# Performance work log

Measured on AMD Instinct MI355X. Metric: run time of the kernel, lower is better.

Reference implementation:

```python
import jax, jax.numpy as jnp
import numpy as np

B, C, D = 512, 1000, 512
K = 10


def setup_inputs() -> dict:
    key = jax.random.key(0)
    k1, k2, k3, k4, k5 = jax.random.split(key, 5)
    x = jax.random.normal(k1, (B, D), dtype=jnp.float32)
    protos = jax.random.normal(k2, (C, D), dtype=jnp.float32)
    # ex2/ex1 chosen so N*ex2^2 - ex1^2 > 0 (valid sqrt)
    ex2 = jax.random.uniform(k3, (C, D), dtype=jnp.float32) + 1.0
    ex1 = jax.random.uniform(k4, (C, D), dtype=jnp.float32) * 0.1
    cls_num = jax.random.randint(k5, (C,), 1, 100, dtype=jnp.int32)
    proto_label = jnp.arange(C, dtype=jnp.int32)
    return {"x": x, "protos": protos, "ex2": ex2, "ex1": ex1,
            "cls_num": cls_num, "proto_label": proto_label, "k_nearest": K}


def reference(x, protos, ex2, ex1, cls_num, proto_label, k_nearest):
    # rd: per-class, per-feature variance proxy  [C, D]
    N = cls_num[:, None].astype(ex2.dtype)
    rd = jnp.sqrt(N * ex2 ** 2 - ex1 ** 2)
    # softmax over feature dim of (rowmax - rd)
    rd = jax.nn.softmax(jnp.max(rd, axis=1, keepdims=True) - rd, axis=1)
    # weighted squared distances: [B, C, D] -> reduce D -> [B, C]
    diff = x[:, None, :] - protos[None, :, :]
    x_dists = diff ** 2 * rd[None, :, :]
    simi_mat = x_dists.sum(axis=2)  # [B, C]
    # k smallest distances (torch.topk largest=False)
    neg_vals, topk_index = jax.lax.top_k(-simi_mat, k_nearest)
    topk_vals = -neg_vals  # [B, K]
    topk_conf = topk_vals.sum(axis=1, keepdims=True) / topk_vals  # [B, K]
    # pick prototype with max confidence, map through label table
    temp = jnp.argmax(topk_conf, axis=1)  # [B]
    ans_index = jnp.take_along_axis(topk_index, temp[:, None], axis=1)[:, 0]
    predict = proto_label[ans_index]  # [B]
    return predict, topk_conf
```

## Files before the change

kernel.cpp:

```cpp
#include <hip/hip_runtime.h>
#include <math.h>
#include <float.h>

#define B_SZ 512
#define C_SZ 1000
#define D_SZ 512
#define K_TOP 10
#define K2 1024
#define NSPLIT 4
#define KSPLIT (K2 / NSPLIT)
#define BC (B_SZ * C_SZ)

#define A_OFF   0
#define W_OFF   (B_SZ * K2)
#define T3_OFF  (W_OFF + C_SZ * K2)
#define PART_OFF (T3_OFF + 1024)

__global__ __launch_bounds__(256) void prep_kernel(const float* __restrict__ x,
                                                   const float* __restrict__ protos,
                                                   const float* __restrict__ ex2,
                                                   const float* __restrict__ ex1,
                                                   const int* __restrict__ cls_num,
                                                   float* __restrict__ ws) {
    float* A  = ws + A_OFF;
    float* W  = ws + W_OFF;
    float* t3 = ws + T3_OFF;
    const int wid  = threadIdx.x >> 6;
    const int lane = threadIdx.x & 63;
    const int blk  = blockIdx.x;

    if (blk < C_SZ / 4) {
        const int c = blk * 4 + wid;
        const size_t rb = (size_t)c * D_SZ + lane * 8;
        float e2v[8], e1v[8], pv[8];
        *(float4*)&e2v[0] = *(const float4*)(ex2 + rb);
        *(float4*)&e2v[4] = *(const float4*)(ex2 + rb + 4);
        *(float4*)&e1v[0] = *(const float4*)(ex1 + rb);
        *(float4*)&e1v[4] = *(const float4*)(ex1 + rb + 4);
        *(float4*)&pv[0]  = *(const float4*)(protos + rb);
        *(float4*)&pv[4]  = *(const float4*)(protos + rb + 4);
        const float N = (float)cls_num[c];

        float v[8], mn = FLT_MAX;
        #pragma unroll
        for (int k = 0; k < 8; k++) {
            v[k] = sqrtf(N * e2v[k] * e2v[k] - e1v[k] * e1v[k]);
            mn = fminf(mn, v[k]);
        }
        #pragma unroll
        for (int off = 1; off < 64; off <<= 1) mn = fminf(mn, __shfl_xor(mn, off));

        float ev[8], s = 0.f;
        #pragma unroll
        for (int k = 0; k < 8; k++) { ev[k] = expf(mn - v[k]); s += ev[k]; }
        #pragma unroll
        for (int off = 1; off < 64; off <<= 1) s += __shfl_xor(s, off);
        const float inv = 1.0f / s;

        float w1[8], w2[8], t = 0.f;
        #pragma unroll
        for (int k = 0; k < 8; k++) {
            const float rdv = ev[k] * inv;
            w1[k] = rdv;
            w2[k] = -2.0f * rdv * pv[k];
            t = fmaf(rdv * pv[k], pv[k], t);
        }
        float* wr = W + (size_t)c * K2 + lane * 8;
        *(float4*)(wr)              = *(float4*)&w1[0];
        *(float4*)(wr + 4)          = *(float4*)&w1[4];
        *(float4*)(wr + D_SZ)       = *(float4*)&w2[0];
        *(float4*)(wr + D_SZ + 4)   = *(float4*)&w2[4];
        #pragma unroll
        for (int off = 1; off < 64; off <<= 1) t += __shfl_xor(t, off);
        if (lane == 0) t3[c] = t;
    } else {
        const int b = (blk - C_SZ / 4) * 4 + wid;
        const size_t rb = (size_t)b * D_SZ + lane * 8;
        float xv[8], xs[8];
        *(float4*)&xv[0] = *(const float4*)(x + rb);
        *(float4*)&xv[4] = *(const float4*)(x + rb + 4);
        #pragma unroll
        for (int k = 0; k < 8; k++) xs[k] = xv[k] * xv[k];
        float* ar = A + (size_t)b * K2 + lane * 8;
        *(float4*)(ar)            = *(float4*)&xs[0];
        *(float4*)(ar + 4)        = *(float4*)&xs[4];
        *(float4*)(ar + D_SZ)     = *(float4*)&xv[0];
        *(float4*)(ar + D_SZ + 4) = *(float4*)&xv[4];
    }
}

#define TM 64
#define TN 64
#define KB 32

__global__ __launch_bounds__(256) void gemm_kernel(const float* __restrict__ A,
                                                   const float* __restrict__ W,
                                                   float* __restrict__ part) {
    __shared__ float as[KB][TM + 4];
    __shared__ float wsm[KB][TN + 4];

    const int tid = threadIdx.x;
    const int tx = tid & 15;
    const int ty = tid >> 4;
    const int c0 = blockIdx.x * TN;
    const int b0 = blockIdx.y * TM;
    const int kz = blockIdx.z;

    float acc[4][4] = {};

    for (int k0 = kz * KSPLIT; k0 < (kz + 1) * KSPLIT; k0 += KB) {
        #pragma unroll
        for (int i = 0; i < 2; i++) {
            const int f = tid + i * 256;
            const int row = f >> 3;
            const int col = (f & 7) * 4;
            float4 va = *(const float4*)(A + (size_t)(b0 + row) * K2 + k0 + col);
            as[col + 0][row] = va.x; as[col + 1][row] = va.y;
            as[col + 2][row] = va.z; as[col + 3][row] = va.w;
            const int cc = c0 + row;
            float4 vw = make_float4(0.f, 0.f, 0.f, 0.f);
            if (cc < C_SZ) vw = *(const float4*)(W + (size_t)cc * K2 + k0 + col);
            wsm[col + 0][row] = vw.x; wsm[col + 1][row] = vw.y;
            wsm[col + 2][row] = vw.z; wsm[col + 3][row] = vw.w;
        }
        __syncthreads();

        #pragma unroll
        for (int kk = 0; kk < KB; kk++) {
            float4 av4 = *(const float4*)&as[kk][ty * 4];
            float4 wv4 = *(const float4*)&wsm[kk][tx * 4];
            const float a[4] = {av4.x, av4.y, av4.z, av4.w};
            const float w[4] = {wv4.x, wv4.y, wv4.z, wv4.w};
            #pragma unroll
            for (int i = 0; i < 4; i++)
                #pragma unroll
                for (int j = 0; j < 4; j++)
                    acc[i][j] = fmaf(a[i], w[j], acc[i][j]);
        }
        __syncthreads();
    }

    float* o = part + (size_t)kz * BC;
    #pragma unroll
    for (int i = 0; i < 4; i++) {
        const int b = b0 + ty * 4 + i;
        const int c = c0 + tx * 4;
        if (c + 3 < C_SZ) {
            float4 v = {acc[i][0], acc[i][1], acc[i][2], acc[i][3]};
            *(float4*)(o + (size_t)b * C_SZ + c) = v;
        } else {
            #pragma unroll
            for (int j = 0; j < 4; j++)
                if (c + j < C_SZ) o[(size_t)b * C_SZ + c + j] = acc[i][j];
        }
    }
}

__global__ __launch_bounds__(256) void topk_kernel(const float* __restrict__ ws,
                                                   const int* __restrict__ proto_label,
                                                   float* __restrict__ out) {
    const float* part = ws + PART_OFF;
    const float* t3   = ws + T3_OFF;
    const int wid = threadIdx.x >> 6;
    const int lane = threadIdx.x & 63;
    const int b = blockIdx.x * 4 + wid;

    float vals[16];
    #pragma unroll
    for (int j = 0; j < 16; j++) {
        const int c = lane + j * 64;
        if (c < C_SZ) {
            const size_t idx = (size_t)b * C_SZ + c;
            vals[j] = t3[c] + part[idx] + part[BC + idx]
                    + part[2 * (size_t)BC + idx] + part[3 * (size_t)BC + idx];
        } else {
            vals[j] = FLT_MAX;
        }
    }

    float kv[K_TOP];
    int ki[K_TOP];
    for (int t = 0; t < K_TOP; t++) {
        float bv = FLT_MAX;
        int bi = 0x7fffffff;
        #pragma unroll
        for (int j = 0; j < 16; j++) {
            const int c = lane + j * 64;
            if (vals[j] < bv) { bv = vals[j]; bi = c; }
        }
        #pragma unroll
        for (int off = 1; off < 64; off <<= 1) {
            const float ov = __shfl_xor(bv, off);
            const int oi = __shfl_xor(bi, off);
            if (ov < bv || (ov == bv && oi < bi)) { bv = ov; bi = oi; }
        }
        kv[t] = bv;
        ki[t] = bi;
        if ((bi & 63) == lane) vals[bi >> 6] = FLT_MAX;
    }

    if (lane == 0) {
        float S = 0.f;
        #pragma unroll
        for (int t = 0; t < K_TOP; t++) S += kv[t];
        float conf[K_TOP];
        #pragma unroll
        for (int t = 0; t < K_TOP; t++) {
            conf[t] = S / kv[t];
            out[B_SZ + b * K_TOP + t] = conf[t];
        }
        int best = 0;
        for (int t = 1; t < K_TOP; t++)
            if (conf[t] > conf[best]) best = t;
        out[b] = (float)proto_label[ki[best]];
    }
}

extern "C" void kernel_launch(void* const* d_in, const int* in_sizes, int n_in,
                              void* d_out, int out_size, void* d_ws, size_t ws_size,
                              hipStream_t stream) {
    const float* x           = (const float*)d_in[0];
    const float* protos      = (const float*)d_in[1];
    const float* ex2         = (const float*)d_in[2];
    const float* ex1         = (const float*)d_in[3];
    const int*   cls_num     = (const int*)d_in[4];
    const int*   proto_label = (const int*)d_in[5];

    float* ws  = (float*)d_ws;
    float* out = (float*)d_out;

    prep_kernel<<<C_SZ / 4 + B_SZ / 4, 256, 0, stream>>>(x, protos, ex2, ex1,
                                                         cls_num, ws);

    dim3 g2((C_SZ + TN - 1) / TN, B_SZ / TM, NSPLIT);
    gemm_kernel<<<g2, 256, 0, stream>>>(ws + A_OFF, ws + W_OFF, ws + PART_OFF);

    topk_kernel<<<B_SZ / 4, 256, 0, stream>>>(ws, proto_label, out);
}
```

Before: 108.3 us.

## Fuse x-squaring into GEMM loads, prefetch tiles, and double split-K

The prep kernel no longer builds the augmented A matrix [x^2 | x]. The GEMM now reads x directly and squares it on the fly for the first half of the K splits, which removes a 2 MB write and re-read through workspace. The GEMM loop also register-prefetches the next chunk of x and W while computing the current one, and split-K goes from 4 to 8 for more blocks. In exchange, the top-k kernel must read and sum twice as many partial buffers.

```diff
diff --git a/kernel.cpp b/kernel.cpp
--- a/kernel.cpp
+++ b/kernel.cpp
@@ -7,94 +7,75 @@
 #define D_SZ 512
 #define K_TOP 10
 #define K2 1024
-#define NSPLIT 4
+#define NSPLIT 8
 #define KSPLIT (K2 / NSPLIT)
 #define BC (B_SZ * C_SZ)
 
-#define A_OFF   0
-#define W_OFF   (B_SZ * K2)
+#define W_OFF   0
 #define T3_OFF  (W_OFF + C_SZ * K2)
 #define PART_OFF (T3_OFF + 1024)
 
-__global__ __launch_bounds__(256) void prep_kernel(const float* __restrict__ x,
-                                                   const float* __restrict__ protos,
+__global__ __launch_bounds__(256) void prep_kernel(const float* __restrict__ protos,
                                                    const float* __restrict__ ex2,
                                                    const float* __restrict__ ex1,
                                                    const int* __restrict__ cls_num,
                                                    float* __restrict__ ws) {
-    float* A  = ws + A_OFF;
     float* W  = ws + W_OFF;
     float* t3 = ws + T3_OFF;
     const int wid  = threadIdx.x >> 6;
     const int lane = threadIdx.x & 63;
-    const int blk  = blockIdx.x;
-
-    if (blk < C_SZ / 4) {
-        const int c = blk * 4 + wid;
-        const size_t rb = (size_t)c * D_SZ + lane * 8;
-        float e2v[8], e1v[8], pv[8];
-        *(float4*)&e2v[0] = *(const float4*)(ex2 + rb);
-        *(float4*)&e2v[4] = *(const float4*)(ex2 + rb + 4);
-        *(float4*)&e1v[0] = *(const float4*)(ex1 + rb);
-        *(float4*)&e1v[4] = *(const float4*)(ex1 + rb + 4);
-        *(float4*)&pv[0]  = *(const float4*)(protos + rb);
-        *(float4*)&pv[4]  = *(const float4*)(protos + rb + 4);
-        const float N = (float)cls_num[c];
-
-        float v[8], mn = FLT_MAX;
-        #pragma unroll
-        for (int k = 0; k < 8; k++) {
-            v[k] = sqrtf(N * e2v[k] * e2v[k] - e1v[k] * e1v[k]);
-            mn = fminf(mn, v[k]);
-        }
-        #pragma unroll
-        for (int off = 1; off < 64; off <<= 1) mn = fminf(mn, __shfl_xor(mn, off));
-
-        float ev[8], s = 0.f;
-        #pragma unroll
-        for (int k = 0; k < 8; k++) { ev[k] = expf(mn - v[k]); s += ev[k]; }
-        #pragma unroll
-        for (int off = 1; off < 64; off <<= 1) s += __shfl_xor(s, off);
-        const float inv = 1.0f / s;
-
-        float w1[8], w2[8], t = 0.f;
-        #pragma unroll
-        for (int k = 0; k < 8; k++) {
-            const float rdv = ev[k] * inv;
-            w1[k] = rdv;
-            w2[k] = -2.0f * rdv * pv[k];
-            t = fmaf(rdv * pv[k], pv[k], t);
-        }
-        float* wr = W + (size_t)c * K2 + lane * 8;
-        *(float4*)(wr)              = *(float4*)&w1[0];
-        *(float4*)(wr + 4)          = *(float4*)&w1[4];
-        *(float4*)(wr + D_SZ)       = *(float4*)&w2[0];
-        *(float4*)(wr + D_SZ + 4)   = *(float4*)&w2[4];
-        #pragma unroll
-        for (int off = 1; off < 64; off <<= 1) t += __shfl_xor(t, off);
-        if (lane == 0) t3[c] = t;
-    } else {
-        const int b = (blk - C_SZ / 4) * 4 + wid;
-        const size_t rb = (size_t)b * D_SZ + lane * 8;
-        float xv[8], xs[8];
-        *(float4*)&xv[0] = *(const float4*)(x + rb);
-        *(float4*)&xv[4] = *(const float4*)(x + rb + 4);
-        #pragma unroll
-        for (int k = 0; k < 8; k++) xs[k] = xv[k] * xv[k];
-        float* ar = A + (size_t)b * K2 + lane * 8;
-        *(float4*)(ar)            = *(float4*)&xs[0];
-        *(float4*)(ar + 4)        = *(float4*)&xs[4];
-        *(float4*)(ar + D_SZ)     = *(float4*)&xv[0];
-        *(float4*)(ar + D_SZ + 4) = *(float4*)&xv[4];
-    }
+    const int c = blockIdx.x * 4 + wid;
+
+    const size_t rb = (size_t)c * D_SZ + lane * 8;
+    float e2v[8], e1v[8], pv[8];
+    *(float4*)&e2v[0] = *(const float4*)(ex2 + rb);
+    *(float4*)&e2v[4] = *(const float4*)(ex2 + rb + 4);
+    *(float4*)&e1v[0] = *(const float4*)(ex1 + rb);
+    *(float4*)&e1v[4] = *(const float4*)(ex1 + rb + 4);
+    *(float4*)&pv[0]  = *(const float4*)(protos + rb);
+    *(float4*)&pv[4]  = *(const float4*)(protos + rb + 4);
+    const float N = (float)cls_num[c];
+
+    float v[8], mn = FLT_MAX;
+    #pragma unroll
+    for (int k = 0; k < 8; k++) {
+        v[k] = sqrtf(N * e2v[k] * e2v[k] - e1v[k] * e1v[k]);
+        mn = fminf(mn, v[k]);
+    }
+    #pragma unroll
+    for (int off = 1; off < 64; off <<= 1) mn = fminf(mn, __shfl_xor(mn, off));
+
+    float ev[8], s = 0.f;
+    #pragma unroll
+    for (int k = 0; k < 8; k++) { ev[k] = expf(mn - v[k]); s += ev[k]; }
+    #pragma unroll
+    for (int off = 1; off < 64; off <<= 1) s += __shfl_xor(s, off);
+    const float inv = 1.0f / s;
+
+    float w1[8], w2[8], t = 0.f;
+    #pragma unroll
+    for (int k = 0; k < 8; k++) {
+        const float rdv = ev[k] * inv;
+        w1[k] = rdv;
+        w2[k] = -2.0f * rdv * pv[k];
+        t = fmaf(rdv * pv[k], pv[k], t);
+    }
+    float* wr = W + (size_t)c * K2 + lane * 8;
+    *(float4*)(wr)            = *(float4*)&w1[0];
+    *(float4*)(wr + 4)        = *(float4*)&w1[4];
+    *(float4*)(wr + D_SZ)     = *(float4*)&w2[0];
+    *(float4*)(wr + D_SZ + 4) = *(float4*)&w2[4];
+    #pragma unroll
+    for (int off = 1; off < 64; off <<= 1) t += __shfl_xor(t, off);
+    if (lane == 0) t3[c] = t;
 }
 
 #define TM 64
 #define TN 64
 #define KB 32
 
-__global__ __launch_bounds__(256) void gemm_kernel(const float* __restrict__ A,
-                                                   const float* __restrict__ W,
+__global__ __launch_bounds__(256) void gemm_kernel(const float* __restrict__ x,
+                                                   const float* __restrict__ Wm,
                                                    float* __restrict__ part) {
     __shared__ float as[KB][TM + 4];
     __shared__ float wsm[KB][TN + 4];
@@ -106,29 +87,59 @@
     const int b0 = blockIdx.y * TM;
     const int kz = blockIdx.z;
 
+    const int row0 = tid >> 3;
+    const int row1 = row0 + 32;
+    const int col4 = (tid & 7) * 4;
+
+    const bool sq = (kz < NSPLIT / 2);
+    const int khalf = sq ? kz * KSPLIT : kz * KSPLIT - D_SZ;
+
     float acc[4][4] = {};
-
-    for (int k0 = kz * KSPLIT; k0 < (kz + 1) * KSPLIT; k0 += KB) {
-        #pragma unroll
-        for (int i = 0; i < 2; i++) {
-            const int f = tid + i * 256;
-            const int row = f >> 3;
-            const int col = (f & 7) * 4;
-            float4 va = *(const float4*)(A + (size_t)(b0 + row) * K2 + k0 + col);
-            as[col + 0][row] = va.x; as[col + 1][row] = va.y;
-            as[col + 2][row] = va.z; as[col + 3][row] = va.w;
-            const int cc = c0 + row;
-            float4 vw = make_float4(0.f, 0.f, 0.f, 0.f);
-            if (cc < C_SZ) vw = *(const float4*)(W + (size_t)cc * K2 + k0 + col);
-            wsm[col + 0][row] = vw.x; wsm[col + 1][row] = vw.y;
-            wsm[col + 2][row] = vw.z; wsm[col + 3][row] = vw.w;
-        }
+    float4 pa0, pa1, pw0, pw1;
+
+    {
+        const int k0 = khalf;
+        pa0 = *(const float4*)(x + (size_t)(b0 + row0) * D_SZ + k0 + col4);
+        pa1 = *(const float4*)(x + (size_t)(b0 + row1) * D_SZ + k0 + col4);
+        const int kw = kz * KSPLIT;
+        const int cc0 = c0 + row0, cc1 = c0 + row1;
+        pw0 = (cc0 < C_SZ) ? *(const float4*)(Wm + (size_t)cc0 * K2 + kw + col4)
+                           : make_float4(0.f, 0.f, 0.f, 0.f);
+        pw1 = (cc1 < C_SZ) ? *(const float4*)(Wm + (size_t)cc1 * K2 + kw + col4)
+                           : make_float4(0.f, 0.f, 0.f, 0.f);
+    }
+
+    #pragma unroll
+    for (int ch = 0; ch < KSPLIT / KB; ch++) {
+        float4 a0 = pa0, a1 = pa1;
+        if (sq) {
+            a0.x *= a0.x; a0.y *= a0.y; a0.z *= a0.z; a0.w *= a0.w;
+            a1.x *= a1.x; a1.y *= a1.y; a1.z *= a1.z; a1.w *= a1.w;
+        }
+        as[col4 + 0][row0] = a0.x; as[col4 + 1][row0] = a0.y;
+        as[col4 + 2][row0] = a0.z; as[col4 + 3][row0] = a0.w;
+        as[col4 + 0][row1] = a1.x; as[col4 + 1][row1] = a1.y;
+        as[col4 + 2][row1] = a1.z; as[col4 + 3][row1] = a1.w;
+        wsm[col4 + 0][row0] = pw0.x; wsm[col4 + 1][row0] = pw0.y;
+        wsm[col4 + 2][row0] = pw0.z; wsm[col4 + 3][row0] = pw0.w;
+        wsm[col4 + 0][row1] = pw1.x; wsm[col4 + 1][row1] = pw1.y;
+        wsm[col4 + 2][row1] = pw1.z; wsm[col4 + 3][row1] = pw1.w;
         __syncthreads();
 
+        if (ch + 1 < KSPLIT / KB) {
+            const int k0 = khalf + (ch + 1) * KB;
+            pa0 = *(const float4*)(x + (size_t)(b0 + row0) * D_SZ + k0 + col4);
+            pa1 = *(const float4*)(x + (size_t)(b0 + row1) * D_SZ + k0 + col4);
+            const int kw = kz * KSPLIT + (ch + 1) * KB;
+            const int cc0 = c0 + row0, cc1 = c0 + row1;
+            if (cc0 < C_SZ) pw0 = *(const float4*)(Wm + (size_t)cc0 * K2 + kw + col4);
+            if (cc1 < C_SZ) pw1 = *(const float4*)(Wm + (size_t)cc1 * K2 + kw + col4);
+        }
+
         #pragma unroll
         for (int kk = 0; kk < KB; kk++) {
-            float4 av4 = *(const float4*)&as[kk][ty * 4];
-            float4 wv4 = *(const float4*)&wsm[kk][tx * 4];
+            const float4 av4 = *(const float4*)&as[kk][ty * 4];
+            const float4 wv4 = *(const float4*)&wsm[kk][tx * 4];
             const float a[4] = {av4.x, av4.y, av4.z, av4.w};
             const float w[4] = {wv4.x, wv4.y, wv4.z, wv4.w};
             #pragma unroll
@@ -171,8 +182,11 @@
         const int c = lane + j * 64;
         if (c < C_SZ) {
             const size_t idx = (size_t)b * C_SZ + c;
-            vals[j] = t3[c] + part[idx] + part[BC + idx]
-                    + part[2 * (size_t)BC + idx] + part[3 * (size_t)BC + idx];
+            float s = t3[c];
+            #pragma unroll
+            for (int z = 0; z < NSPLIT; z++)
+                s += part[(size_t)z * BC + idx];
+            vals[j] = s;
         } else {
             vals[j] = FLT_MAX;
         }
@@ -229,11 +243,10 @@
     float* ws  = (float*)d_ws;
     float* out = (float*)d_out;
 
-    prep_kernel<<<C_SZ / 4 + B_SZ / 4, 256, 0, stream>>>(x, protos, ex2, ex1,
-                                                         cls_num, ws);
+    prep_kernel<<<C_SZ / 4, 256, 0, stream>>>(protos, ex2, ex1, cls_num, ws);
 
     dim3 g2((C_SZ + TN - 1) / TN, B_SZ / TM, NSPLIT);
-    gemm_kernel<<<g2, 256, 0, stream>>>(ws + A_OFF, ws + W_OFF, ws + PART_OFF);
+    gemm_kernel<<<g2, 256, 0, stream>>>(x, ws + W_OFF, ws + PART_OFF);
 
     topk_kernel<<<B_SZ / 4, 256, 0, stream>>>(ws, proto_label, out);
 }
```

Measured after the change: 296.4 us. +173.8%, slower.
